# Performance work log

Measured on AMD Instinct MI355X. Metric: run time of the kernel, lower is better.

## Reference

```python
import jax, jax.numpy as jnp
import numpy as np

NB, NR = 100000, 200000            # bridge / road node counts
E_BR, E_RB, E_BB = 1000000, 1000000, 500000  # edges per relation
H = 32                             # hidden_channels


def _sage(h_src, h_dst, src, dst, n_dst, Wl, bl, Wr):
    # PyG SAGEConv: lin_l(mean_{j in N(i)} x_j) + lin_r(x_i); lin_r has no bias
    msg = jnp.take(h_src, src, axis=0)                      # [E, H] gather
    s = jax.ops.segment_sum(msg, dst, num_segments=n_dst)   # [n_dst, H] scatter-add
    cnt = jax.ops.segment_sum(jnp.ones((dst.shape[0],), h_src.dtype), dst, num_segments=n_dst)
    mean = s / jnp.maximum(cnt, 1.0)[:, None]                # mean aggregation
    return mean @ Wl + bl + h_dst @ Wr


def setup_inputs():
    key = jax.random.key(0)
    ks = jax.random.split(key, 24)
    n = lambda i, shape, s=0.1: jax.random.normal(ks[i], shape, jnp.float32) * s
    return {
        "x_bridge": n(0, (NB, 16), 1.0),
        "x_road": n(1, (NR, 8), 1.0),
        "src_br": jax.random.randint(ks[2], (E_BR,), 0, NB),
        "dst_br": jax.random.randint(ks[3], (E_BR,), 0, NR),
        "src_rb": jax.random.randint(ks[4], (E_RB,), 0, NR),
        "dst_rb": jax.random.randint(ks[5], (E_RB,), 0, NB),
        "src_bb": jax.random.randint(ks[6], (E_BB,), 0, NB),
        "dst_bb": jax.random.randint(ks[7], (E_BB,), 0, NB),
        "W_enc_b": n(8, (16, H)), "b_enc_b": n(9, (H,)),
        "W_enc_r": n(10, (8, H)), "b_enc_r": n(11, (H,)),
        "Wl_br": n(12, (H, H)), "bl_br": n(13, (H,)), "Wr_br": n(14, (H, H)),
        "Wl_rb": n(15, (H, H)), "bl_rb": n(16, (H,)), "Wr_rb": n(17, (H, H)),
        "Wl_bb": n(18, (H, H)), "bl_bb": n(19, (H,)), "Wr_bb": n(20, (H, H)),
        "Wo": n(21, (H, 1)), "bo": n(22, (1,)),
    }


def reference(x_bridge, x_road, src_br, dst_br, src_rb, dst_rb, src_bb, dst_bb,
              W_enc_b, b_enc_b, W_enc_r, b_enc_r,
              Wl_br, bl_br, Wr_br, Wl_rb, bl_rb, Wr_rb, Wl_bb, bl_bb, Wr_bb,
              Wo, bo):
    # per-node-type encoder + relu
    h_b = jax.nn.relu(x_bridge @ W_enc_b + b_enc_b)          # [NB, H]
    h_r = jax.nn.relu(x_road @ W_enc_r + b_enc_r)            # [NR, H]
    # HeteroConv(aggr='sum'): 'bridge' receives road->bridge and bridge->bridge.
    # (bridge->road output is dead code w.r.t. the returned bridge head; XLA DCEs it.)
    out_b = (_sage(h_r, h_b, src_rb, dst_rb, NB, Wl_rb, bl_rb, Wr_rb)
             + _sage(h_b, h_b, src_bb, dst_bb, NB, Wl_bb, bl_bb, Wr_bb))
    # relu then output Linear on 'bridge'
    return jax.nn.relu(out_b) @ Wo + bo                       # [NB, 1]
```

## Files before the change

kernel.cpp:

```cpp
#include <hip/hip_runtime.h>
#include <hip/hip_fp16.h>

#define H 32
#define TPB 256
#define EPT 32
#define SLOTS 128
#define CAP 2048
#define MAXBUCK 2048

__global__ void __launch_bounds__(TPB) prep_kernel(
        const float* __restrict__ x_b, const float* __restrict__ x_r,
        const float* __restrict__ W_b, const float* __restrict__ b_b,
        const float* __restrict__ W_r, const float* __restrict__ b_r,
        __half* __restrict__ h_b16, __half* __restrict__ h_r16,
        int NB, int NR, int encBlocks,
        const int* __restrict__ src_rb, const int* __restrict__ dst_rb,
        const int* __restrict__ src_bb, const int* __restrict__ dst_bb,
        int* __restrict__ gcurp, int* __restrict__ bins,
        int E_RB, int E_BB, int NBUCK) {
    int t = threadIdx.x;

    if (blockIdx.x < encBlocks) {
        __shared__ float sWb[16][H];
        __shared__ float sWr8[8][H];
        __shared__ float sbb[H];
        __shared__ float sbr[H];
        for (int i = t; i < 16 * H; i += TPB) ((float*)sWb)[i] = W_b[i];
        for (int i = t; i < 8 * H; i += TPB) ((float*)sWr8)[i] = W_r[i];
        if (t < H) { sbb[t] = b_b[t]; sbr[t] = b_r[t]; }
        __syncthreads();

        long long node = (long long)blockIdx.x * TPB + t;
        if (node < NB) {
            const float4* px = (const float4*)(x_b + node * 16);
            float acc[H];
            #pragma unroll
            for (int j = 0; j < H; ++j) acc[j] = sbb[j];
            #pragma unroll
            for (int c = 0; c < 4; ++c) {
                float4 q = px[c];
                float xs[4] = {q.x, q.y, q.z, q.w};
                #pragma unroll
                for (int u = 0; u < 4; ++u) {
                    int k = c * 4 + u;
                    #pragma unroll
                    for (int j = 0; j < H; ++j)
                        acc[j] = fmaf(xs[u], sWb[k][j], acc[j]);
                }
            }
            __half2 o[H / 2];
            #pragma unroll
            for (int j2 = 0; j2 < H / 2; ++j2)
                o[j2] = __floats2half2_rn(fmaxf(acc[2 * j2], 0.0f), fmaxf(acc[2 * j2 + 1], 0.0f));
            float4* dst = (float4*)(h_b16 + node * H);
            const float4* src = (const float4*)o;
            dst[0] = src[0]; dst[1] = src[1]; dst[2] = src[2]; dst[3] = src[3];
        } else if (node < (long long)NB + NR) {
            long long m = node - NB;
            const float4* px = (const float4*)(x_r + m * 8);
            float acc[H];
            #pragma unroll
            for (int j = 0; j < H; ++j) acc[j] = sbr[j];
            #pragma unroll
            for (int c = 0; c < 2; ++c) {
                float4 q = px[c];
                float xs[4] = {q.x, q.y, q.z, q.w};
                #pragma unroll
                for (int u = 0; u < 4; ++u) {
                    int k = c * 4 + u;
                    #pragma unroll
                    for (int j = 0; j < H; ++j)
                        acc[j] = fmaf(xs[u], sWr8[k][j], acc[j]);
                }
            }
            __half2 o[H / 2];
            #pragma unroll
            for (int j2 = 0; j2 < H / 2; ++j2)
                o[j2] = __floats2half2_rn(fmaxf(acc[2 * j2], 0.0f), fmaxf(acc[2 * j2 + 1], 0.0f));
            float4* dst = (float4*)(h_r16 + m * H);
            const float4* src = (const float4*)o;
            dst[0] = src[0]; dst[1] = src[1]; dst[2] = src[2]; dst[3] = src[3];
        }
    } else {
        __shared__ int lcnt[MAXBUCK];
        __shared__ int wbase[MAXBUCK];
        for (int i = t; i < MAXBUCK; i += TPB) lcnt[i] = 0;
        __syncthreads();

        long long e0 = (long long)(blockIdx.x - encBlocks) * (TPB * EPT);
        long long EA = (long long)E_RB + E_BB;
        long long rb4 = (long long)(E_RB >> 2);
        int meta[EPT];

        #pragma unroll
        for (int j = 0; j < EPT / 4; ++j) {
            long long i4 = (e0 >> 2) + (long long)j * TPB + t;
            long long eb = i4 << 2;
            int dd[4];
            if (eb + 3 < (long long)E_RB) {
                int4 dv = ((const int4*)dst_rb)[i4];
                dd[0] = dv.x; dd[1] = dv.y; dd[2] = dv.z; dd[3] = dv.w;
            } else if (eb >= (long long)E_RB && eb + 3 < EA) {
                int4 dv = ((const int4*)dst_bb)[i4 - rb4];
                dd[0] = dv.x + NB; dd[1] = dv.y + NB; dd[2] = dv.z + NB; dd[3] = dv.w + NB;
            } else {
                #pragma unroll
                for (int u = 0; u < 4; ++u) {
                    long long e = eb + u;
                    dd[u] = (e < E_RB) ? dst_rb[e] : (e < EA ? NB + dst_bb[e - E_RB] : -1);
                }
            }
            #pragma unroll
            for (int u = 0; u < 4; ++u) {
                if (dd[u] >= 0) {
                    int bk = dd[u] >> 7;
                    int loc = atomicAdd(&lcnt[bk], 1);
                    meta[j * 4 + u] = (bk << 20) | (loc << 7) | (dd[u] & 127);
                } else meta[j * 4 + u] = -1;
            }
        }
        __syncthreads();

        for (int i = t; i < NBUCK; i += TPB) {
            int c = lcnt[i];
            wbase[i] = c ? (i * CAP + atomicAdd(&gcurp[i * 16], c)) : 0;
        }
        __syncthreads();

        #pragma unroll
        for (int j = 0; j < EPT / 4; ++j) {
            long long i4 = (e0 >> 2) + (long long)j * TPB + t;
            long long eb = i4 << 2;
            int ss[4];
            if (eb + 3 < (long long)E_RB) {
                int4 sv = ((const int4*)src_rb)[i4];
                ss[0] = sv.x; ss[1] = sv.y; ss[2] = sv.z; ss[3] = sv.w;
            } else if (eb >= (long long)E_RB && eb + 3 < EA) {
                int4 sv = ((const int4*)src_bb)[i4 - rb4];
                ss[0] = sv.x; ss[1] = sv.y; ss[2] = sv.z; ss[3] = sv.w;
            } else {
                #pragma unroll
                for (int u = 0; u < 4; ++u) {
                    long long e = eb + u;
                    ss[u] = (e < E_RB) ? src_rb[e] : (e < EA ? (int)src_bb[e - E_RB] : 0);
                }
            }
            #pragma unroll
            for (int u = 0; u < 4; ++u) {
                int m = meta[j * 4 + u];
                if (m >= 0) {
                    int bk = (unsigned)m >> 20;
                    int loc = (m >> 7) & 0x1FFF;
                    int dloc = m & 127;
                    int gslot = wbase[bk] + loc;
                    if (gslot < (bk + 1) * CAP)
                        bins[gslot] = (ss[u] << 7) | dloc;
                }
            }
        }
    }
}

__global__ void __launch_bounds__(TPB) buildgather_kernel(
        const __half* __restrict__ h_r16, const __half* __restrict__ h_b16,
        const int* __restrict__ bins, const int* __restrict__ gcurp,
        __half* __restrict__ mean16, int NB, int N2) {
    __shared__ int rawbuf[CAP];
    __shared__ int srcbuf[CAP];
    __shared__ int lcnt[SLOTS];
    __shared__ int lbase[SLOTS];
    __shared__ int lcur[SLOTS];
    __shared__ int tmp[SLOTS];
    int t = threadIdx.x;
    int b = blockIdx.x;
    int start = b * CAP;
    int n = gcurp[b * 16];
    if (n > CAP) n = CAP;

    if (t < SLOTS) lcnt[t] = 0;
    __syncthreads();

    {
        int n4 = n >> 2;
        const int4* bins4 = (const int4*)(bins + start);
        for (int i = t; i < n4; i += TPB) {
            int4 p = bins4[i];
            ((int4*)rawbuf)[i] = p;
            atomicAdd(&lcnt[p.x & 127], 1);
            atomicAdd(&lcnt[p.y & 127], 1);
            atomicAdd(&lcnt[p.z & 127], 1);
            atomicAdd(&lcnt[p.w & 127], 1);
        }
        for (int i = (n4 << 2) + t; i < n; i += TPB) {
            int packed = bins[start + i];
            rawbuf[i] = packed;
            atomicAdd(&lcnt[packed & 127], 1);
        }
    }
    __syncthreads();

    if (t < SLOTS) tmp[t] = lcnt[t];
    __syncthreads();
    for (int off = 1; off < SLOTS; off <<= 1) {
        int x = (t >= off && t < SLOTS) ? tmp[t - off] : 0;
        __syncthreads();
        if (t < SLOTS) tmp[t] += x;
        __syncthreads();
    }
    if (t < SLOTS) { lbase[t] = tmp[t] - lcnt[t]; lcur[t] = tmp[t] - lcnt[t]; }
    __syncthreads();

    for (int i = t; i < n; i += TPB) {
        int packed = rawbuf[i];
        int slot = atomicAdd(&lcur[packed & 127], 1);
        srcbuf[slot] = packed >> 7;
    }
    __syncthreads();

    int lane = t & 15, g = t >> 4;
    long long base_slot = (long long)b << 7;
    for (int sl = g; sl < SLOTS; sl += (TPB / 16)) {
        long long gd = base_slot + sl;
        if (gd >= N2) break;
        const __half* __restrict__ hs = (gd < NB) ? h_r16 : h_b16;
        int off = lbase[sl];
        int cnt = lcnt[sl];
        float ax = 0.0f, ay = 0.0f;
        int k = 0;
        for (; k + 8 <= cnt; k += 8) {
            int s[8];
            #pragma unroll
            for (int j = 0; j < 8; ++j) s[j] = srcbuf[off + k + j];
            float2 f[8];
            #pragma unroll
            for (int j = 0; j < 8; ++j)
                f[j] = __half22float2(*(const __half2*)(hs + (long long)s[j] * H + 2 * lane));
            #pragma unroll
            for (int j = 0; j < 8; ++j) { ax += f[j].x; ay += f[j].y; }
        }
        if (k + 4 <= cnt) {
            int s[4];
            #pragma unroll
            for (int j = 0; j < 4; ++j) s[j] = srcbuf[off + k + j];
            float2 f[4];
            #pragma unroll
            for (int j = 0; j < 4; ++j)
                f[j] = __half22float2(*(const __half2*)(hs + (long long)s[j] * H + 2 * lane));
            #pragma unroll
            for (int j = 0; j < 4; ++j) { ax += f[j].x; ay += f[j].y; }
            k += 4;
        }
        for (; k < cnt; ++k) {
            int s = srcbuf[off + k];
            float2 f = __half22float2(*(const __half2*)(hs + (long long)s * H + 2 * lane));
            ax += f.x; ay += f.y;
        }
        float inv = 1.0f / fmaxf((float)cnt, 1.0f);
        *(__half2*)(mean16 + gd * H + 2 * lane) = __floats2half2_rn(ax * inv, ay * inv);
    }
}

__global__ void __launch_bounds__(TPB) head_kernel(
        const __half* __restrict__ h_b16,
        const __half* __restrict__ mean16,
        const float* __restrict__ Wl_rb,
        const float* __restrict__ bl_rb,
        const float* __restrict__ Wl_bb,
        const float* __restrict__ bl_bb,
        const float* __restrict__ Wr_rb,
        const float* __restrict__ Wr_bb,
        const float* __restrict__ Wo,
        const float* __restrict__ bo,
        float* __restrict__ y, int N) {
    __shared__ float sWl_rb[H][H];
    __shared__ float sWl_bb[H][H];
    __shared__ float sWr[H][H];
    __shared__ float sbl[H];
    __shared__ float sWo[H];
    __shared__ float sbo;

    int t = threadIdx.x;
    for (int i = t; i < H * H; i += blockDim.x) {
        ((float*)sWl_rb)[i] = Wl_rb[i];
        ((float*)sWl_bb)[i] = Wl_bb[i];
        ((float*)sWr)[i]    = Wr_rb[i] + Wr_bb[i];
    }
    if (t < H) {
        sbl[t] = bl_rb[t] + bl_bb[t];
        sWo[t] = Wo[t];
    }
    if (t == 0) sbo = bo[0];
    __syncthreads();

    int node = blockIdx.x * TPB + t;
    if (node >= N) return;

    const float4* pr = (const float4*)(mean16 + (long long)node * H);
    const float4* pb = (const float4*)(mean16 + ((long long)N + node) * H);
    const float4* ph = (const float4*)(h_b16 + (long long)node * H);

    float acc[H];
    #pragma unroll
    for (int j = 0; j < H; ++j) acc[j] = sbl[j];

    #pragma unroll
    for (int c = 0; c < 4; ++c) {
        float4 qr = pr[c];
        float4 qb = pb[c];
        float4 qh = ph[c];
        const __half2* hr = (const __half2*)&qr;
        const __half2* hb = (const __half2*)&qb;
        const __half2* hh = (const __half2*)&qh;
        #pragma unroll
        for (int u = 0; u < 4; ++u) {
            float2 fr = __half22float2(hr[u]);
            float2 fb = __half22float2(hb[u]);
            float2 fh = __half22float2(hh[u]);
            int k0 = c * 8 + u * 2;
            #pragma unroll
            for (int j = 0; j < H; ++j) {
                acc[j] = fmaf(fr.x, sWl_rb[k0][j], acc[j]);
                acc[j] = fmaf(fb.x, sWl_bb[k0][j], acc[j]);
                acc[j] = fmaf(fh.x, sWr[k0][j], acc[j]);
                acc[j] = fmaf(fr.y, sWl_rb[k0 + 1][j], acc[j]);
                acc[j] = fmaf(fb.y, sWl_bb[k0 + 1][j], acc[j]);
                acc[j] = fmaf(fh.y, sWr[k0 + 1][j], acc[j]);
            }
        }
    }

    float out = 0.0f;
    #pragma unroll
    for (int j = 0; j < H; ++j)
        out = fmaf(fmaxf(acc[j], 0.0f), sWo[j], out);
    y[node] = out + sbo;
}

extern "C" void kernel_launch(void* const* d_in, const int* in_sizes, int n_in,
                              void* d_out, int out_size, void* d_ws, size_t ws_size,
                              hipStream_t stream) {
    const float* x_bridge = (const float*)d_in[0];
    const float* x_road   = (const float*)d_in[1];
    const int* src_rb = (const int*)d_in[4];
    const int* dst_rb = (const int*)d_in[5];
    const int* src_bb = (const int*)d_in[6];
    const int* dst_bb = (const int*)d_in[7];
    const float* W_enc_b = (const float*)d_in[8];
    const float* b_enc_b = (const float*)d_in[9];
    const float* W_enc_r = (const float*)d_in[10];
    const float* b_enc_r = (const float*)d_in[11];
    const float* Wl_rb = (const float*)d_in[15];
    const float* bl_rb = (const float*)d_in[16];
    const float* Wr_rb = (const float*)d_in[17];
    const float* Wl_bb = (const float*)d_in[18];
    const float* bl_bb = (const float*)d_in[19];
    const float* Wr_bb = (const float*)d_in[20];
    const float* Wo = (const float*)d_in[21];
    const float* bo = (const float*)d_in[22];
    float* y = (float*)d_out;

    const int NB = in_sizes[0] / 16;
    const int NR = in_sizes[1] / 8;
    const int E_RB = in_sizes[4];
    const int E_BB = in_sizes[6];
    const int N2 = 2 * NB;
    const long long E_ALL = (long long)E_RB + E_BB;
    const int NBUCK = (N2 + SLOTS - 1) / SLOTS;

    char* wp = (char*)d_ws;
    __half* h_r16  = (__half*)wp; wp += (size_t)NR * H * sizeof(__half);
    __half* h_b16  = (__half*)wp; wp += (size_t)NB * H * sizeof(__half);
    __half* mean16 = (__half*)wp; wp += (size_t)N2 * H * sizeof(__half);
    int* bins  = (int*)wp;       wp += (size_t)NBUCK * CAP * sizeof(int);
    int* gcurp = (int*)wp;       wp += (size_t)NBUCK * 16 * sizeof(int);

    hipMemsetAsync(gcurp, 0, (size_t)NBUCK * 16 * sizeof(int), stream);

    long long nodes = (long long)NB + NR;
    int encBlocks = (int)((nodes + TPB - 1) / TPB);
    int placeBlocks = (int)((E_ALL + (TPB * EPT) - 1) / (TPB * EPT));
    prep_kernel<<<encBlocks + placeBlocks, TPB, 0, stream>>>(
        x_bridge, x_road, W_enc_b, b_enc_b, W_enc_r, b_enc_r,
        h_b16, h_r16, NB, NR, encBlocks,
        src_rb, dst_rb, src_bb, dst_bb, gcurp, bins, E_RB, E_BB, NBUCK);

    buildgather_kernel<<<NBUCK, TPB, 0, stream>>>(h_r16, h_b16, bins, gcurp,
                                                  mean16, NB, N2);

    head_kernel<<<(NB + TPB - 1) / TPB, TPB, 0, stream>>>(h_b16, mean16,
                                                  Wl_rb, bl_rb, Wl_bb, bl_bb,
                                                  Wr_rb, Wr_bb, Wo, bo, y, NB);
}
```

Before: 95.23 us.

## Split edge bucketing into two-pass radix placement via superbuckets

Edge placement now bins edges first into coarse superbuckets of 2048 destinations, which replaces the 2048-entry per-block shared histogram and its per-bucket global atomics. A new placeB kernel then splits each superbucket into 16 fine buckets of 128 slots for the existing gather kernel. EPT is halved to give more placement blocks. The intent is to cut shared-memory init and scan work and global atomic contention in the first pass. The cost is an extra kernel launch and an extra read/write pass over all edges.

New measurement: 94.86 us. About the same (-0.4%).

```diff
diff --git a/kernel.cpp b/kernel.cpp
--- a/kernel.cpp
+++ b/kernel.cpp
@@ -3,10 +3,13 @@
 
 #define H 32
 #define TPB 256
-#define EPT 32
+#define EPT 16
 #define SLOTS 128
 #define CAP 2048
-#define MAXBUCK 2048
+#define SUPB 2048
+#define CAP1 22528
+#define K2 4
+#define NSUPMAX 128
 
 __global__ void __launch_bounds__(TPB) prep_kernel(
         const float* __restrict__ x_b, const float* __restrict__ x_r,
@@ -16,8 +19,8 @@
         int NB, int NR, int encBlocks,
         const int* __restrict__ src_rb, const int* __restrict__ dst_rb,
         const int* __restrict__ src_bb, const int* __restrict__ dst_bb,
-        int* __restrict__ gcurp, int* __restrict__ bins,
-        int E_RB, int E_BB, int NBUCK) {
+        int* __restrict__ gcur1, int* __restrict__ bins1,
+        int E_RB, int E_BB, int NSUP) {
     int t = threadIdx.x;
 
     if (blockIdx.x < encBlocks) {
@@ -82,9 +85,9 @@
             dst[0] = src[0]; dst[1] = src[1]; dst[2] = src[2]; dst[3] = src[3];
         }
     } else {
-        __shared__ int lcnt[MAXBUCK];
-        __shared__ int wbase[MAXBUCK];
-        for (int i = t; i < MAXBUCK; i += TPB) lcnt[i] = 0;
+        __shared__ int lcnt[NSUPMAX];
+        __shared__ int wbase[NSUPMAX];
+        if (t < NSUPMAX) { lcnt[t] = 0; }
         __syncthreads();
 
         long long e0 = (long long)(blockIdx.x - encBlocks) * (TPB * EPT);
@@ -113,17 +116,17 @@
             #pragma unroll
             for (int u = 0; u < 4; ++u) {
                 if (dd[u] >= 0) {
-                    int bk = dd[u] >> 7;
-                    int loc = atomicAdd(&lcnt[bk], 1);
-                    meta[j * 4 + u] = (bk << 20) | (loc << 7) | (dd[u] & 127);
+                    int sup = dd[u] >> 11;
+                    int loc = atomicAdd(&lcnt[sup], 1);
+                    meta[j * 4 + u] = (sup << 23) | (loc << 11) | (dd[u] & 2047);
                 } else meta[j * 4 + u] = -1;
             }
         }
         __syncthreads();
 
-        for (int i = t; i < NBUCK; i += TPB) {
-            int c = lcnt[i];
-            wbase[i] = c ? (i * CAP + atomicAdd(&gcurp[i * 16], c)) : 0;
+        if (t < NSUP) {
+            int c = lcnt[t];
+            wbase[t] = c ? (t * CAP1 + atomicAdd(&gcur1[t * 16], c)) : 0;
         }
         __syncthreads();
 
@@ -149,21 +152,62 @@
             for (int u = 0; u < 4; ++u) {
                 int m = meta[j * 4 + u];
                 if (m >= 0) {
-                    int bk = (unsigned)m >> 20;
-                    int loc = (m >> 7) & 0x1FFF;
-                    int dloc = m & 127;
-                    int gslot = wbase[bk] + loc;
-                    if (gslot < (bk + 1) * CAP)
-                        bins[gslot] = (ss[u] << 7) | dloc;
+                    int sup = (unsigned)m >> 23;
+                    int loc = (m >> 11) & 0xFFF;
+                    int gslot = wbase[sup] + loc;
+                    if (gslot < (sup + 1) * CAP1)
+                        bins1[gslot] = (ss[u] << 11) | (m & 2047);
                 }
             }
         }
+    }
+}
+
+__global__ void __launch_bounds__(TPB) placeB_kernel(
+        const int* __restrict__ bins1, const int* __restrict__ gcur1,
+        int* __restrict__ gcur2, int* __restrict__ bins, int NBUCK) {
+    __shared__ int lcnt[16];
+    __shared__ int wbase[16];
+    __shared__ int lcur[16];
+    int t = threadIdx.x;
+    int sup = blockIdx.x / K2;
+    int j   = blockIdx.x % K2;
+    int n = gcur1[sup * 16];
+    if (n > CAP1) n = CAP1;
+    int chunk = (n + K2 - 1) / K2;
+    int lo = j * chunk;
+    int hi = lo + chunk; if (hi > n) hi = n;
+
+    if (t < 16) lcnt[t] = 0;
+    __syncthreads();
+
+    const int* __restrict__ seg = bins1 + (long long)sup * CAP1;
+    for (int i = lo + t; i < hi; i += TPB)
+        atomicAdd(&lcnt[(seg[i] >> 7) & 15], 1);
+    __syncthreads();
+
+    if (t < 16) {
+        int c = lcnt[t];
+        int fb = sup * 16 + t;
+        wbase[t] = (c && fb < NBUCK) ? (fb * CAP + atomicAdd(&gcur2[fb * 16], c)) : 0;
+        lcur[t] = 0;
+    }
+    __syncthreads();
+
+    for (int i = lo + t; i < hi; i += TPB) {
+        int p = seg[i];
+        int f = (p >> 7) & 15;
+        int loc = atomicAdd(&lcur[f], 1);
+        int fb = sup * 16 + f;
+        int gslot = wbase[f] + loc;
+        if (gslot < (fb + 1) * CAP)
+            bins[gslot] = ((p >> 11) << 7) | (p & 127);
     }
 }
 
 __global__ void __launch_bounds__(TPB) buildgather_kernel(
         const __half* __restrict__ h_r16, const __half* __restrict__ h_b16,
-        const int* __restrict__ bins, const int* __restrict__ gcurp,
+        const int* __restrict__ bins, const int* __restrict__ gcur2,
         __half* __restrict__ mean16, int NB, int N2) {
     __shared__ int rawbuf[CAP];
     __shared__ int srcbuf[CAP];
@@ -174,7 +218,7 @@
     int t = threadIdx.x;
     int b = blockIdx.x;
     int start = b * CAP;
-    int n = gcurp[b * 16];
+    int n = gcur2[b * 16];
     if (n > CAP) n = CAP;
 
     if (t < SLOTS) lcnt[t] = 0;
@@ -230,24 +274,24 @@
         for (; k + 8 <= cnt; k += 8) {
             int s[8];
             #pragma unroll
-            for (int j = 0; j < 8; ++j) s[j] = srcbuf[off + k + j];
+            for (int jj = 0; jj < 8; ++jj) s[jj] = srcbuf[off + k + jj];
             float2 f[8];
             #pragma unroll
-            for (int j = 0; j < 8; ++j)
-                f[j] = __half22float2(*(const __half2*)(hs + (long long)s[j] * H + 2 * lane));
-            #pragma unroll
-            for (int j = 0; j < 8; ++j) { ax += f[j].x; ay += f[j].y; }
+            for (int jj = 0; jj < 8; ++jj)
+                f[jj] = __half22float2(*(const __half2*)(hs + (long long)s[jj] * H + 2 * lane));
+            #pragma unroll
+            for (int jj = 0; jj < 8; ++jj) { ax += f[jj].x; ay += f[jj].y; }
         }
         if (k + 4 <= cnt) {
             int s[4];
             #pragma unroll
-            for (int j = 0; j < 4; ++j) s[j] = srcbuf[off + k + j];
+            for (int jj = 0; jj < 4; ++jj) s[jj] = srcbuf[off + k + jj];
             float2 f[4];
             #pragma unroll
-            for (int j = 0; j < 4; ++j)
-                f[j] = __half22float2(*(const __half2*)(hs + (long long)s[j] * H + 2 * lane));
-            #pragma unroll
-            for (int j = 0; j < 4; ++j) { ax += f[j].x; ay += f[j].y; }
+            for (int jj = 0; jj < 4; ++jj)
+                f[jj] = __half22float2(*(const __half2*)(hs + (long long)s[jj] * H + 2 * lane));
+            #pragma unroll
+            for (int jj = 0; jj < 4; ++jj) { ax += f[jj].x; ay += f[jj].y; }
             k += 4;
         }
         for (; k < cnt; ++k) {
@@ -366,15 +410,18 @@
     const int N2 = 2 * NB;
     const long long E_ALL = (long long)E_RB + E_BB;
     const int NBUCK = (N2 + SLOTS - 1) / SLOTS;
+    const int NSUP  = (N2 + SUPB - 1) / SUPB;
 
     char* wp = (char*)d_ws;
     __half* h_r16  = (__half*)wp; wp += (size_t)NR * H * sizeof(__half);
     __half* h_b16  = (__half*)wp; wp += (size_t)NB * H * sizeof(__half);
     __half* mean16 = (__half*)wp; wp += (size_t)N2 * H * sizeof(__half);
+    int* bins1 = (int*)wp;       wp += (size_t)NSUP * CAP1 * sizeof(int);
     int* bins  = (int*)wp;       wp += (size_t)NBUCK * CAP * sizeof(int);
-    int* gcurp = (int*)wp;       wp += (size_t)NBUCK * 16 * sizeof(int);
-
-    hipMemsetAsync(gcurp, 0, (size_t)NBUCK * 16 * sizeof(int), stream);
+    int* gcur1 = (int*)wp;       wp += (size_t)NSUP * 16 * sizeof(int);
+    int* gcur2 = (int*)wp;       wp += (size_t)NBUCK * 16 * sizeof(int);
+
+    hipMemsetAsync(gcur1, 0, (size_t)(NSUP + NBUCK) * 16 * sizeof(int), stream);
 
     long long nodes = (long long)NB + NR;
     int encBlocks = (int)((nodes + TPB - 1) / TPB);
@@ -382,9 +429,11 @@
     prep_kernel<<<encBlocks + placeBlocks, TPB, 0, stream>>>(
         x_bridge, x_road, W_enc_b, b_enc_b, W_enc_r, b_enc_r,
         h_b16, h_r16, NB, NR, encBlocks,
-        src_rb, dst_rb, src_bb, dst_bb, gcurp, bins, E_RB, E_BB, NBUCK);
-
-    buildgather_kernel<<<NBUCK, TPB, 0, stream>>>(h_r16, h_b16, bins, gcurp,
+        src_rb, dst_rb, src_bb, dst_bb, gcur1, bins1, E_RB, E_BB, NSUP);
+
+    placeB_kernel<<<NSUP * K2, TPB, 0, stream>>>(bins1, gcur1, gcur2, bins, NBUCK);
+
+    buildgather_kernel<<<NBUCK, TPB, 0, stream>>>(h_r16, h_b16, bins, gcur2,
                                                   mean16, NB, N2);
 
     head_kernel<<<(NB + TPB - 1) / TPB, TPB, 0, stream>>>(h_b16, mean16,
```
